# Kernel tuning notes

Measured on AMD Instinct MI355X. Metric: run time of the kernel, lower is better.

The kernel has to match this reference:

```python
import jax, jax.numpy as jnp
import numpy as np

N_NODES = 100000
N_EDGES = 1600000
N_GRAPHS = 1024
DIM_IN = 128
DIM_SELF = 16
BN_EPS = 1e-5


def _bn(x, gamma, beta):
    # training-mode BatchNorm1d over dim 0 (biased variance, as torch uses for normalization)
    m = jnp.mean(x, axis=0)
    v = jnp.mean((x - m) ** 2, axis=0)
    return gamma * (x - m) * jax.lax.rsqrt(v + BN_EPS) + beta


def _mlp(x, W1, b1, g, b, W2, b2):
    h = x @ W1 + b1
    h = jax.nn.relu(_bn(h, g, b))
    return h @ W2 + b2


def _gin(h, src, dst, W1, b1, g, b, W2, b2):
    # GINConv with eps=0: (1+eps)*h + sum over in-neighbors, then MLP
    agg = jax.ops.segment_sum(h[src], dst, num_segments=N_NODES)
    return _mlp(h + agg, W1, b1, g, b, W2, b2)


def setup_inputs() -> dict:
    key = jax.random.key(0)
    ks = jax.random.split(key, 16)

    def lin(k, fan_in, fan_out):
        bound = 1.0 / np.sqrt(fan_in)
        k1, k2 = jax.random.split(k)
        W = jax.random.uniform(k1, (fan_in, fan_out), jnp.float32, -bound, bound)
        b = jax.random.uniform(k2, (fan_out,), jnp.float32, -bound, bound)
        return W, b

    inp = {}
    inp['feat'] = jax.random.normal(ks[0], (N_NODES, DIM_IN), jnp.float32)
    inp['self_feat'] = jax.random.normal(ks[1], (N_GRAPHS, DIM_SELF), jnp.float32)
    inp['edge_src'] = jax.random.randint(ks[2], (N_EDGES,), 0, N_NODES, jnp.int32)
    inp['edge_dst'] = jax.random.randint(ks[3], (N_EDGES,), 0, N_NODES, jnp.int32)
    inp['node2graph'] = jnp.sort(jax.random.randint(ks[4], (N_NODES,), 0, N_GRAPHS, jnp.int32))

    inp['g1_W1'], inp['g1_b1'] = lin(ks[5], DIM_IN, 100)
    inp['g1_gamma'] = jnp.ones((100,), jnp.float32)
    inp['g1_beta'] = jnp.zeros((100,), jnp.float32)
    inp['g1_W2'], inp['g1_b2'] = lin(ks[6], 100, 100)

    inp['g2_W1'], inp['g2_b1'] = lin(ks[7], 100, 20)
    inp['g2_gamma'] = jnp.ones((20,), jnp.float32)
    inp['g2_beta'] = jnp.zeros((20,), jnp.float32)
    inp['g2_W2'], inp['g2_b2'] = lin(ks[8], 20, 20)

    inp['fc1_W'], inp['fc1_b'] = lin(ks[9], 20 * DIM_SELF, 32)
    inp['bn1_gamma'] = jnp.ones((32,), jnp.float32)
    inp['bn1_beta'] = jnp.zeros((32,), jnp.float32)
    inp['fc2_W'], inp['fc2_b'] = lin(ks[10], 32, 8)
    inp['bn2_gamma'] = jnp.ones((8,), jnp.float32)
    inp['bn2_beta'] = jnp.zeros((8,), jnp.float32)
    inp['fc3_W'], inp['fc3_b'] = lin(ks[11], 8, 1)
    return inp


def reference(feat, self_feat,
              g1_W1, g1_b1, g1_gamma, g1_beta, g1_W2, g1_b2,
              g2_W1, g2_b1, g2_gamma, g2_beta, g2_W2, g2_b2,
              fc1_W, fc1_b, bn1_gamma, bn1_beta,
              fc2_W, fc2_b, bn2_gamma, bn2_beta,
              fc3_W, fc3_b,
              edge_src, edge_dst, node2graph):
    h = _gin(feat, edge_src, edge_dst, g1_W1, g1_b1, g1_gamma, g1_beta, g1_W2, g1_b2)
    h = jax.nn.relu(h)
    h = _gin(h, edge_src, edge_dst, g2_W1, g2_b1, g2_gamma, g2_beta, g2_W2, g2_b2)
    h = jax.nn.relu(h)  # [N, 20]

    # dgl.mean_nodes: per-graph mean of node features
    sums = jax.ops.segment_sum(h, node2graph, num_segments=N_GRAPHS)  # [B, 20]
    cnts = jax.ops.segment_sum(jnp.ones((N_NODES,), h.dtype), node2graph, num_segments=N_GRAPHS)
    hg = sums / jnp.maximum(cnts, 1.0)[:, None]

    # kronecker fusion: bmm([B,20,1],[B,1,dim_self]) -> flatten
    kron = jnp.einsum('bi,bj->bij', hg, self_feat).reshape(N_GRAPHS, -1)  # [B, 20*dim_self]

    out = jax.nn.relu(_bn(kron @ fc1_W + fc1_b, bn1_gamma, bn1_beta))
    # dropout(0.3) is identity in eval mode
    out = jax.nn.relu(_bn(out @ fc2_W + fc2_b, bn2_gamma, bn2_beta))
    out = out @ fc3_W + fc3_b  # [B, dim_out]
    return out
```

## Files before the change

### kernel.cpp

```cpp
#include <hip/hip_runtime.h>

#define NN 100000
#define NE 1600000
#define NG 1024
#define DIN 128
#define D1 100
#define D2 20
#define DSELF 16
#define BN_EPS 1e-5f

#define NB 391
#define NBLK 782
#define EPB 2048
#define RAWCAP 5120
#define NAGG2 4000
#define NF1 25
#define NF2 40
#define APITCH 136

typedef unsigned int uint;
typedef unsigned short ushort;
typedef __attribute__((ext_vector_type(8))) short bfv8;
typedef __attribute__((ext_vector_type(4))) float fv4;

__device__ inline float bflo(uint x) { return __uint_as_float(x << 16); }
__device__ inline float bfhi(uint x) { return __uint_as_float(x & 0xffff0000u); }
__device__ inline uint packbf2(float a, float b) {
    uint ua = __float_as_uint(a), ub = __float_as_uint(b);
    ua += 0x7fffu + ((ua >> 16) & 1u);
    ub += 0x7fffu + ((ub >> 16) & 1u);
    return (ua >> 16) | (ub & 0xffff0000u);
}
__device__ inline ushort bfr(float x) {
    uint u = __float_as_uint(x);
    u += 0x7fffu + ((u >> 16) & 1u);
    return (ushort)(u >> 16);
}

__global__ __launch_bounds__(256) void k_gemm1(const float* __restrict__ feat,
                                               const float* __restrict__ W1,
                                               ushort* __restrict__ z1bf) {
    __shared__ __align__(16) char smem[64 * APITCH * 2 + 112 * APITCH * 2];
    ushort* Al = (ushort*)smem;
    ushort* Bt = (ushort*)(smem + 64 * APITCH * 2);
    int t = threadIdx.x;
    int row0 = blockIdx.x * 64;
#pragma unroll
    for (int i = 0; i < 8; i++) {
        int p = i * 256 + t;
        int r = p >> 5, cq = p & 31;
        int row = row0 + r; if (row >= NN) row = NN - 1;
        float4 v = *(const float4*)(feat + (size_t)row * DIN + cq * 4);
        ushort* dst = Al + r * APITCH + 4 * cq;
        dst[0] = bfr(v.x); dst[1] = bfr(v.y); dst[2] = bfr(v.z); dst[3] = bfr(v.w);
    }
    for (int p = t; p < 12800; p += 256) {
        int k = p / 100, n = p % 100;
        Bt[n * APITCH + k] = bfr(W1[p]);
    }
    __syncthreads();
    int w = __builtin_amdgcn_readfirstlane(t >> 6);
    int l = t & 63;
    int m16 = l & 15, quad = l >> 4;
    fv4 acc[7];
#pragma unroll
    for (int nt = 0; nt < 7; nt++) acc[nt] = (fv4){0.f, 0.f, 0.f, 0.f};
    const ushort* arow = Al + (w * 16 + m16) * APITCH;
#pragma unroll
    for (int kk = 0; kk < 4; kk++) {
        int kb = kk * 32 + quad * 8;
        bfv8 a = *(const bfv8*)(arow + kb);
#pragma unroll
        for (int nt = 0; nt < 7; nt++) {
            bfv8 b = *(const bfv8*)(Bt + (nt * 16 + m16) * APITCH + kb);
            acc[nt] = __builtin_amdgcn_mfma_f32_16x16x32_bf16(a, b, acc[nt], 0, 0, 0);
        }
    }
    __syncthreads();
    float* Ep = (float*)smem;
#pragma unroll
    for (int nt = 0; nt < 7; nt++) {
        int n = nt * 16 + m16;
        if (n < 100) {
#pragma unroll
            for (int rix = 0; rix < 4; rix++)
                Ep[(w * 16 + quad * 4 + rix) * 101 + n] = acc[nt][rix];
        }
    }
    __syncthreads();
#pragma unroll
    for (int i = 0; i < 13; i++) {
        int p = i * 256 + t;
        if (p < 3200) {
            int rr = p / 50, cc = 2 * (p % 50);
            int row = row0 + rr;
            if (row < NN) {
                float v0 = Ep[rr * 101 + cc], v1 = Ep[rr * 101 + cc + 1];
                *(uint*)(z1bf + (size_t)row * 128 + cc) = packbf2(v0, v1);
            }
        }
    }
}

__global__ __launch_bounds__(256) void k_csrA1(const int* __restrict__ dst,
                                               int* __restrict__ pbcount) {
    __shared__ int h[NB];
    int t = threadIdx.x, blk = blockIdx.x;
    for (int i = t; i < NB; i += 256) h[i] = 0;
    __syncthreads();
    int e0 = blk * EPB + t;
#pragma unroll
    for (int i = 0; i < 8; i++) {
        int e = e0 + i * 256;
        if (e < NE) atomicAdd(&h[dst[e] >> 8], 1);
    }
    __syncthreads();
    for (int i = t; i < NB; i += 256) pbcount[i * NBLK + blk] = h[i];
}

__global__ __launch_bounds__(1024) void k_csrS1(int* __restrict__ pbcount,
                                                int* __restrict__ btot) {
    __shared__ int s[1024];
    int t = threadIdx.x, b = blockIdx.x;
    int v = (t < NBLK) ? pbcount[b * NBLK + t] : 0;
    s[t] = v;
    __syncthreads();
    for (int off = 1; off < 1024; off <<= 1) {
        int x = (t >= off) ? s[t - off] : 0;
        __syncthreads();
        s[t] += x;
        __syncthreads();
    }
    if (t < NBLK) pbcount[b * NBLK + t] = s[t] - v;
    if (t == 1023) btot[b] = s[t];
}

__global__ __launch_bounds__(256) void k_csrA2(const int* __restrict__ src,
                                               const int* __restrict__ dst,
                                               const int* __restrict__ pbexcl,
                                               const int* __restrict__ btot,
                                               int* __restrict__ ebase_g,
                                               uint* __restrict__ gbuf) {
    __shared__ int cur[NB];
    __shared__ int sa[512], sb[512];
    int t = threadIdx.x, blk = blockIdx.x;
    int o0 = (t < NB) ? btot[t] : 0;
    int o1 = (t + 256 < NB) ? btot[t + 256] : 0;
    sa[t] = o0; sa[t + 256] = o1;
    __syncthreads();
    int* sp = sa; int* dp = sb;
    for (int off = 1; off < 512; off <<= 1) {
        dp[t] = sp[t] + ((t >= off) ? sp[t - off] : 0);
        int i2 = t + 256;
        dp[i2] = sp[i2] + ((i2 >= off) ? sp[i2 - off] : 0);
        __syncthreads();
        int* tmp = sp; sp = dp; dp = tmp;
    }
    if (t < NB)       cur[t]       = (sp[t] - o0) + pbexcl[t * NBLK + blk];
    if (t + 256 < NB) cur[t + 256] = (sp[t + 256] - o1) + pbexcl[(t + 256) * NBLK + blk];
    if (blk == 0) {
        if (t < NB)       ebase_g[t]       = sp[t] - o0;
        if (t + 256 < NB) ebase_g[t + 256] = sp[t + 256] - o1;
        if (t == 0)       ebase_g[NB]      = sp[NB - 1];
    }
    __syncthreads();
    int e0 = blk * EPB + t;
#pragma unroll
    for (int i = 0; i < 8; i++) {
        int e = e0 + i * 256;
        if (e < NE) {
            int d = dst[e];
            int b = d >> 8;
            int pos = atomicAdd(&cur[b], 1);
            gbuf[pos] = (uint)src[e] | ((uint)(d & 255) << 17);
        }
    }
}

__global__ __launch_bounds__(256) void k_csrB(const uint* __restrict__ gbuf,
                                              const int* __restrict__ ebase,
                                              int* __restrict__ deg,
                                              int* __restrict__ offs,
                                              int* __restrict__ srcS) {
    __shared__ uint raw[RAWCAP];
    __shared__ int srt[RAWCAP];
    __shared__ int pref[256], cur[256];
    int t = threadIdx.x, b = blockIdx.x;
    int e0 = ebase[b], e1 = ebase[b + 1];
    int cnt = e1 - e0; if (cnt > RAWCAP) cnt = RAWCAP;
    cur[t] = 0;
    for (int i = t; i < cnt; i += 256) raw[i] = gbuf[e0 + i];
    __syncthreads();
    for (int i = t; i < cnt; i += 256) atomicAdd(&cur[raw[i] >> 17], 1);
    __syncthreads();
    int v = cur[t];
    pref[t] = v;
    __syncthreads();
    for (int off = 1; off < 256; off <<= 1) {
        int x = (t >= off) ? pref[t - off] : 0;
        __syncthreads();
        pref[t] += x;
        __syncthreads();
    }
    int excl = pref[t] - v;
    int node = b * 256 + t;
    if (node < NN) { deg[node] = v; offs[node] = e0 + excl; }
    cur[t] = excl;
    __syncthreads();
    for (int i = t; i < cnt; i += 256) {
        uint p = raw[i];
        int lpos = atomicAdd(&cur[p >> 17], 1);
        srt[lpos] = (int)(p & 0x1FFFFu);
    }
    __syncthreads();
    for (int i = t; i < cnt; i += 256) srcS[e0 + i] = srt[i];
}

__global__ __launch_bounds__(256) void k_agg1(const ushort* __restrict__ z1bf,
                                              const int* __restrict__ offs,
                                              const int* __restrict__ deg,
                                              const int* __restrict__ srcS,
                                              ushort* __restrict__ u1b) {
    int wq = __builtin_amdgcn_readfirstlane(threadIdx.x >> 6);
    int l = threadIdx.x & 63;
    int n = blockIdx.x * 4 + wq;
    if (n >= NN) return;
    int d = deg[n], base = offs[n];
    bool act = l < 50;
    const ushort* zc = z1bf + 2 * l;
    float a0 = 0.f, a1 = 0.f, b0 = 0.f, b1 = 0.f;
    float c0 = 0.f, c1 = 0.f, e0 = 0.f, e1 = 0.f;
    int i = 0;
    for (; i + 8 <= d; i += 8) {
        int s0 = srcS[base + i],     s1 = srcS[base + i + 1];
        int s2 = srcS[base + i + 2], s3 = srcS[base + i + 3];
        int s4 = srcS[base + i + 4], s5 = srcS[base + i + 5];
        int s6 = srcS[base + i + 6], s7 = srcS[base + i + 7];
        if (act) {
            uint x0 = *(const uint*)(zc + (size_t)s0 * 128);
            uint x1 = *(const uint*)(zc + (size_t)s1 * 128);
            uint x2 = *(const uint*)(zc + (size_t)s2 * 128);
            uint x3 = *(const uint*)(zc + (size_t)s3 * 128);
            uint x4 = *(const uint*)(zc + (size_t)s4 * 128);
            uint x5 = *(const uint*)(zc + (size_t)s5 * 128);
            uint x6 = *(const uint*)(zc + (size_t)s6 * 128);
            uint x7 = *(const uint*)(zc + (size_t)s7 * 128);
            a0 += bflo(x0); a1 += bfhi(x0);
            b0 += bflo(x1); b1 += bfhi(x1);
            c0 += bflo(x2); c1 += bfhi(x2);
            e0 += bflo(x3); e1 += bfhi(x3);
            a0 += bflo(x4); a1 += bfhi(x4);
            b0 += bflo(x5); b1 += bfhi(x5);
            c0 += bflo(x6); c1 += bfhi(x6);
            e0 += bflo(x7); e1 += bfhi(x7);
        }
    }
    for (; i + 2 <= d; i += 2) {
        int s0 = srcS[base + i], s1 = srcS[base + i + 1];
        if (act) {
            uint x0 = *(const uint*)(zc + (size_t)s0 * 128);
            uint x1 = *(const uint*)(zc + (size_t)s1 * 128);
            a0 += bflo(x0); a1 += bfhi(x0);
            b0 += bflo(x1); b1 += bfhi(x1);
        }
    }
    if (i < d) {
        int s0 = srcS[base + i];
        if (act) {
            uint x0 = *(const uint*)(zc + (size_t)s0 * 128);
            a0 += bflo(x0); a1 += bfhi(x0);
        }
    }
    if (act) {
        uint xs = *(const uint*)(zc + (size_t)n * 128);
        float r0 = (a0 + b0) + (c0 + e0) + bflo(xs);
        float r1 = (a1 + b1) + (c1 + e1) + bfhi(xs);
        *(uint*)(u1b + (size_t)n * 100 + 2 * l) = packbf2(r0, r1);
    }
}

__global__ __launch_bounds__(256) void k_bnstat100(const ushort* __restrict__ u1b,
                                                   float* __restrict__ pb) {
    __shared__ float ls[10][100], lq[10][100];
    int t = threadIdx.x;
    int r0 = blockIdx.x * 200;
    int r1 = r0 + 200; if (r1 > NN) r1 = NN;
    if (t < 250) {
        int sub = t / 25, q = t % 25;
        float4 S = make_float4(0, 0, 0, 0), Q = make_float4(0, 0, 0, 0);
        for (int r = r0 + sub; r < r1; r += 10) {
            uint2 x = *(const uint2*)(u1b + (size_t)r * 100 + 4 * q);
            float v0 = bflo(x.x), v1 = bfhi(x.x), v2 = bflo(x.y), v3 = bfhi(x.y);
            S.x += v0; S.y += v1; S.z += v2; S.w += v3;
            Q.x = fmaf(v0, v0, Q.x); Q.y = fmaf(v1, v1, Q.y);
            Q.z = fmaf(v2, v2, Q.z); Q.w = fmaf(v3, v3, Q.w);
        }
        ls[sub][4 * q + 0] = S.x; ls[sub][4 * q + 1] = S.y;
        ls[sub][4 * q + 2] = S.z; ls[sub][4 * q + 3] = S.w;
        lq[sub][4 * q + 0] = Q.x; lq[sub][4 * q + 1] = Q.y;
        lq[sub][4 * q + 2] = Q.z; lq[sub][4 * q + 3] = Q.w;
    }
    __syncthreads();
    if (t < 100) {
        float S = 0.f, Q = 0.f;
#pragma unroll
        for (int s = 0; s < 10; s++) { S += ls[s][t]; Q += lq[s][t]; }
        pb[blockIdx.x * 200 + t] = S;
        pb[blockIdx.x * 200 + 100 + t] = Q;
    }
}

__global__ __launch_bounds__(256) void k_fold100(const float* __restrict__ pb,
                                                 float* __restrict__ pbf) {
    __shared__ float ls[4000];
    int t = threadIdx.x, b = blockIdx.x;
    for (int i = t; i < 4000; i += 256) ls[i] = pb[b * 4000 + i];
    __syncthreads();
    if (t < 200) {
        float S = 0.f;
#pragma unroll
        for (int j = 0; j < 20; j++) S += ls[j * 200 + t];
        pbf[b * 200 + t] = S;
    }
}

__global__ __launch_bounds__(512) void k_bnfin100(const float* __restrict__ pbf,
                                                  const float* __restrict__ gamma,
                                                  const float* __restrict__ beta,
                                                  float* __restrict__ sc,
                                                  float* __restrict__ sh) {
    __shared__ float ls[4][100], lq[4][100];
    int t = threadIdx.x;
    if (t < 400) {
        int sub = t / 100, c = t % 100;
        float S = 0.f, Q = 0.f;
        for (int b = sub; b < NF1; b += 4) {
            S += pbf[b * 200 + c];
            Q += pbf[b * 200 + 100 + c];
        }
        ls[sub][c] = S; lq[sub][c] = Q;
    }
    __syncthreads();
    if (t < 100) {
        float S = ls[0][t] + ls[1][t] + ls[2][t] + ls[3][t];
        float Q = lq[0][t] + lq[1][t] + lq[2][t] + lq[3][t];
        float mean = S * (1.f / NN);
        float var = Q * (1.f / NN) - mean * mean;
        float inv = rsqrtf(var + BN_EPS);
        float s = gamma[t] * inv;
        sc[t] = s;
        sh[t] = beta[t] - mean * s;
    }
}

__global__ __launch_bounds__(256) void k_m2(const ushort* __restrict__ u1b,
                                            const float* __restrict__ sc,
                                            const float* __restrict__ sh,
                                            const float* __restrict__ W2,
                                            const float* __restrict__ b2,
                                            const float* __restrict__ W1p,
                                            ushort* __restrict__ z2bf) {
    __shared__ float Xs[100 * 65];
    int t = threadIdx.x;
    int row0 = blockIdx.x * 64;
#pragma unroll
    for (int i = 0; i < 13; i++) {
        int p = i * 256 + t;
        if (p < 3200) {
            int r = p / 50, c = 2 * (p % 50);
            int row = row0 + r; if (row >= NN) row = NN - 1;
            uint x = *(const uint*)(u1b + (size_t)row * 100 + c);
            Xs[c * 65 + r] = fmaxf(bflo(x) * sc[c] + sh[c], 0.f);
            Xs[(c + 1) * 65 + r] = fmaxf(bfhi(x) * sc[c + 1] + sh[c + 1], 0.f);
        }
    }
    __syncthreads();
    int cg = __builtin_amdgcn_readfirstlane(t >> 6);
    int r = t & 63;
    int j0 = cg * 25;
    float H[25];
#pragma unroll
    for (int m = 0; m < 25; m++) H[m] = 0.f;
    for (int k = 0; k < D1; k++) {
        float a = Xs[k * 65 + r];
        const float* wr = W2 + k * D1 + j0;
#pragma unroll
        for (int m = 0; m < 25; m++) H[m] = fmaf(a, wr[m], H[m]);
    }
#pragma unroll
    for (int m = 0; m < 25; m++) H[m] = fmaxf(H[m] + b2[j0 + m], 0.f);
    float pz[20];
#pragma unroll
    for (int c = 0; c < 20; c++) pz[c] = 0.f;
#pragma unroll
    for (int m = 0; m < 25; m++) {
        const float* wp = W1p + (j0 + m) * D2;
#pragma unroll
        for (int c = 0; c < 20; c++) pz[c] = fmaf(H[m], wp[c], pz[c]);
    }
    __syncthreads();
    float* red = Xs;
#pragma unroll
    for (int c = 0; c < 20; c++) red[t * 20 + c] = pz[c];
    __syncthreads();
#pragma unroll
    for (int i = 0; i < 3; i++) {
        int p = i * 256 + t;
        if (p < 640) {
            int rr = p / 10, c2 = 2 * (p % 10);
            int row = row0 + rr;
            if (row < NN) {
                float v0 = red[rr * 20 + c2] + red[(64 + rr) * 20 + c2] +
                           red[(128 + rr) * 20 + c2] + red[(192 + rr) * 20 + c2];
                float v1 = red[rr * 20 + c2 + 1] + red[(64 + rr) * 20 + c2 + 1] +
                           red[(128 + rr) * 20 + c2 + 1] + red[(192 + rr) * 20 + c2 + 1];
                *(uint*)(z2bf + (size_t)row * 32 + c2) = packbf2(v0, v1);
            }
        }
    }
}

__global__ __launch_bounds__(256) void k_agg2(const ushort* __restrict__ z2bf,
                                              const int* __restrict__ offs,
                                              const int* __restrict__ deg,
                                              const int* __restrict__ srcS,
                                              float* __restrict__ u2,
                                              float* __restrict__ pb) {
    __shared__ float ls[500], lq[500];
    int t = threadIdx.x;
    int n = blockIdx.x * 25 + t / 10;
    int c2 = 2 * (t % 10);
    float r0 = 0.f, r1 = 0.f;
    if (t < 250 && n < NN) {
        int d = deg[n], base = offs[n];
        const ushort* zc = z2bf + c2;
        float a0 = 0.f, a1 = 0.f, b0 = 0.f, b1 = 0.f;
        int i = 0;
        for (; i + 2 <= d; i += 2) {
            uint x0 = *(const uint*)(zc + (size_t)srcS[base + i] * 32);
            uint x1 = *(const uint*)(zc + (size_t)srcS[base + i + 1] * 32);
            a0 += bflo(x0); a1 += bfhi(x0);
            b0 += bflo(x1); b1 += bfhi(x1);
        }
        if (i < d) {
            uint x0 = *(const uint*)(zc + (size_t)srcS[base + i] * 32);
            a0 += bflo(x0); a1 += bfhi(x0);
        }
        uint xs = *(const uint*)(zc + (size_t)n * 32);
        r0 = a0 + b0 + bflo(xs);
        r1 = a1 + b1 + bfhi(xs);
        *(float2*)(u2 + (size_t)n * D2 + c2) = make_float2(r0, r1);
    }
    if (t < 250) {
        int idx = (t / 10) * 20 + c2;
        ls[idx] = r0;     lq[idx] = r0 * r0;
        ls[idx + 1] = r1; lq[idx + 1] = r1 * r1;
    }
    __syncthreads();
    if (t < 20) {
        float S = 0.f, Q = 0.f;
#pragma unroll
        for (int j = 0; j < 25; j++) { S += ls[j * 20 + t]; Q += lq[j * 20 + t]; }
        pb[blockIdx.x * 40 + t] = S;
        pb[blockIdx.x * 40 + 20 + t] = Q;
    }
}

__global__ __launch_bounds__(256) void k_fold20(const float* __restrict__ pb,
                                                float* __restrict__ pbf) {
    __shared__ float ls[4000];
    int t = threadIdx.x, b = blockIdx.x;
    for (int i = t; i < 4000; i += 256) ls[i] = pb[b * 4000 + i];
    __syncthreads();
    if (t < 40) {
        float S = 0.f;
#pragma unroll
        for (int j = 0; j < 100; j++) S += ls[j * 40 + t];
        pbf[b * 40 + t] = S;
    }
}

__global__ __launch_bounds__(512) void k_bnfin20(const float* __restrict__ pbf,
                                                 const float* __restrict__ gamma,
                                                 const float* __restrict__ beta,
                                                 float* __restrict__ sc,
                                                 float* __restrict__ sh) {
    __shared__ float ls[25][20], lq[25][20];
    int t = threadIdx.x;
    if (t < 500) {
        int sub = t / 20, c = t % 20;
        float S = 0.f, Q = 0.f;
        for (int b = sub; b < NF2; b += 25) {
            S += pbf[b * 40 + c];
            Q += pbf[b * 40 + 20 + c];
        }
        ls[sub][c] = S; lq[sub][c] = Q;
    }
    __syncthreads();
    if (t < 20) {
        float S = 0.f, Q = 0.f;
#pragma unroll
        for (int s = 0; s < 25; s++) { S += ls[s][t]; Q += lq[s][t]; }
        float mean = S * (1.f / NN);
        float var = Q * (1.f / NN) - mean * mean;
        float inv = rsqrtf(var + BN_EPS);
        float s = gamma[t] * inv;
        sc[t] = s;
        sh[t] = beta[t] - mean * s;
    }
}

__global__ __launch_bounds__(256) void k_m3(const float* __restrict__ u2,
                                            const float* __restrict__ sc,
                                            const float* __restrict__ sh,
                                            const float* __restrict__ W2p,
                                            const float* __restrict__ b2p,
                                            float* __restrict__ h2) {
    int row = blockIdx.x * 256 + threadIdx.x;
    if (row >= NN) return;
    float ya[20];
    const float4* up = (const float4*)(u2 + (size_t)row * D2);
#pragma unroll
    for (int i = 0; i < 5; i++) {
        float4 v = up[i];
        float4 S = *(const float4*)(sc + 4 * i);
        float4 H = *(const float4*)(sh + 4 * i);
        ya[4 * i + 0] = fmaxf(v.x * S.x + H.x, 0.f);
        ya[4 * i + 1] = fmaxf(v.y * S.y + H.y, 0.f);
        ya[4 * i + 2] = fmaxf(v.z * S.z + H.z, 0.f);
        ya[4 * i + 3] = fmaxf(v.w * S.w + H.w, 0.f);
    }
    float hrow[D2];
#pragma unroll
    for (int j = 0; j < D2; j++) {
        float h = b2p[j];
#pragma unroll
        for (int k = 0; k < D2; k++) h = fmaf(ya[k], W2p[k * D2 + j], h);
        hrow[j] = fmaxf(h, 0.f);
    }
    float* hr = h2 + (size_t)row * D2;
#pragma unroll
    for (int c = 0; c < D2; c += 4) {
        float4 o; o.x = hrow[c]; o.y = hrow[c + 1]; o.z = hrow[c + 2]; o.w = hrow[c + 3];
        *(float4*)(hr + c) = o;
    }
}

__global__ __launch_bounds__(256) void k_pool(const float* __restrict__ h2,
                                              const int* __restrict__ n2g,
                                              float* __restrict__ hg) {
    int wq = __builtin_amdgcn_readfirstlane(threadIdx.x >> 6);
    int l = threadIdx.x & 63;
    int g = blockIdx.x * 4 + wq;
    if (g >= NG) return;
    int lo = 0, hi = NN;
    while (lo < hi) { int mid = (lo + hi) >> 1; if (n2g[mid] < g) lo = mid + 1; else hi = mid; }
    int s0 = lo;
    hi = NN;
    while (lo < hi) { int mid = (lo + hi) >> 1; if (n2g[mid] < g + 1) lo = mid + 1; else hi = mid; }
    int s1 = lo;
    float a = 0.f;
    if (l < 60) {
        int rg = l / 20, c = l % 20;
        for (int n = s0 + rg; n < s1; n += 3) a += h2[(size_t)n * D2 + c];
    }
    float v1 = __shfl(a, l + 20, 64);
    float v2 = __shfl(a, l + 40, 64);
    if (l < 20) {
        float cnt = (float)(s1 - s0);
        hg[g * D2 + l] = (a + v1 + v2) / fmaxf(cnt, 1.f);
    }
}

__global__ void k_head1(const float* __restrict__ hg, const float* __restrict__ sf,
                        const float* __restrict__ fc1W, float* __restrict__ a1) {
    int b = blockIdx.x * 8 + threadIdx.x / 32;
    int c = threadIdx.x % 32;
    if (b >= NG) return;
    const float* hgb = hg + b * D2;
    const float* sfb = sf + b * DSELF;
    float acc = 0.f;
    for (int i = 0; i < D2; i++) {
        float hi = hgb[i];
#pragma unroll
        for (int j = 0; j < DSELF; j++)
            acc += hi * sfb[j] * fc1W[(i * DSELF + j) * 32 + c];
    }
    a1[b * 32 + c] = acc;
}

__global__ __launch_bounds__(1024) void k_head2(
    const float* __restrict__ a1, const float* __restrict__ g1,
    const float* __restrict__ be1, const float* __restrict__ fc2W,
    const float* __restrict__ g2, const float* __restrict__ be2,
    const float* __restrict__ fc3W, const float* __restrict__ fc3b,
    float* __restrict__ out) {
    int t = threadIdx.x;
    int lane = t & 63, w = t >> 6;
    __shared__ float s1[16][32], s2[16][32];
    __shared__ float sc[32], sh[32], sc2[8], sh2[8];
    float x[32];
    const float4* ap = (const float4*)(a1 + t * 32);
#pragma unroll
    for (int i = 0; i < 8; i++) {
        float4 v = ap[i];
        x[4 * i] = v.x; x[4 * i + 1] = v.y; x[4 * i + 2] = v.z; x[4 * i + 3] = v.w;
    }
#pragma unroll
    for (int c = 0; c < 32; c++) {
        float v = x[c], q = v * v;
        for (int o = 32; o > 0; o >>= 1) {
            v += __shfl_down(v, o, 64);
            q += __shfl_down(q, o, 64);
        }
        if (lane == 0) { s1[w][c] = v; s2[w][c] = q; }
    }
    __syncthreads();
    if (t < 32) {
        float s = 0.f, q = 0.f;
        for (int ww = 0; ww < 16; ww++) { s += s1[ww][t]; q += s2[ww][t]; }
        float mean = s * (1.f / NG);
        float var = q * (1.f / NG) - mean * mean;
        float inv = rsqrtf(var + BN_EPS);
        float scl = g1[t] * inv;
        sc[t] = scl;
        sh[t] = be1[t] - mean * scl;
    }
    __syncthreads();
#pragma unroll
    for (int c = 0; c < 32; c++) x[c] = fmaxf(x[c] * sc[c] + sh[c], 0.f);
    float y[8];
#pragma unroll
    for (int p = 0; p < 8; p++) {
        float a = 0.f;
#pragma unroll
        for (int c = 0; c < 32; c++) a += x[c] * fc2W[c * 8 + p];
        y[p] = a;
    }
    __syncthreads();
#pragma unroll
    for (int p = 0; p < 8; p++) {
        float v = y[p], q = v * v;
        for (int o = 32; o > 0; o >>= 1) {
            v += __shfl_down(v, o, 64);
            q += __shfl_down(q, o, 64);
        }
        if (lane == 0) { s1[w][p] = v; s2[w][p] = q; }
    }
    __syncthreads();
    if (t < 8) {
        float s = 0.f, q = 0.f;
        for (int ww = 0; ww < 16; ww++) { s += s1[ww][t]; q += s2[ww][t]; }
        float mean = s * (1.f / NG);
        float var = q * (1.f / NG) - mean * mean;
        float inv = rsqrtf(var + BN_EPS);
        float scl = g2[t] * inv;
        sc2[t] = scl;
        sh2[t] = be2[t] - mean * scl;
    }
    __syncthreads();
    float o = fc3b[0];
#pragma unroll
    for (int p = 0; p < 8; p++) {
        float yy = fmaxf(y[p] * sc2[p] + sh2[p], 0.f);
        o += yy * fc3W[p];
    }
    out[t] = o;
}

extern "C" void kernel_launch(void* const* d_in, const int* in_sizes, int n_in,
                              void* d_out, int out_size, void* d_ws, size_t ws_size,
                              hipStream_t stream) {
    const float* feat    = (const float*)d_in[0];
    const float* sf      = (const float*)d_in[1];
    const int*   esrc    = (const int*)d_in[2];
    const int*   edst    = (const int*)d_in[3];
    const int*   n2g     = (const int*)d_in[4];
    const float* g1W1    = (const float*)d_in[5];
    const float* g1gam   = (const float*)d_in[7];
    const float* g1bet   = (const float*)d_in[8];
    const float* g1W2    = (const float*)d_in[9];
    const float* g1b2    = (const float*)d_in[10];
    const float* g2W1    = (const float*)d_in[11];
    const float* g2gam   = (const float*)d_in[13];
    const float* g2bet   = (const float*)d_in[14];
    const float* g2W2    = (const float*)d_in[15];
    const float* g2b2    = (const float*)d_in[16];
    const float* fc1W    = (const float*)d_in[17];
    const float* hbn1g   = (const float*)d_in[19];
    const float* hbn1b   = (const float*)d_in[20];
    const float* fc2W    = (const float*)d_in[21];
    const float* hbn2g   = (const float*)d_in[23];
    const float* hbn2b   = (const float*)d_in[24];
    const float* fc3W    = (const float*)d_in[25];
    const float* fc3b    = (const float*)d_in[26];
    float* out = (float*)d_out;

    char* w = (char*)d_ws;
    size_t off = 0;
    auto alloc = [&](size_t bytes) -> char* {
        char* p = w + off;
        off += (bytes + 15) & ~(size_t)15;
        return p;
    };
    char* regA = alloc((size_t)NN * 128 * 2);
    ushort* z1bf = (ushort*)regA;
    ushort* z2bf = (ushort*)regA;
    float*  u2   = (float*)(regA + 6400000);
    float*  h2   = (float*)(regA + 14400000);
    ushort* u1b  = (ushort*)alloc((size_t)NN * 100 * 2);
    int*   pbcnt = (int*)alloc((size_t)NB * NBLK * 4);
    int*   btot  = (int*)alloc(NB * 4);
    int*   ebase = (int*)alloc((NB + 1) * 4);
    uint*  gbuf  = (uint*)alloc((size_t)NE * 4);
    int*   deg   = (int*)alloc(NN * 4);
    int*   offs  = (int*)alloc(NN * 4);
    int*   srcS  = (int*)alloc((size_t)NE * 4);
    float* pb1   = (float*)alloc(500 * 200 * 4);
    float* pb1f  = (float*)alloc(NF1 * 200 * 4);
    float* pb2   = (float*)alloc((size_t)NAGG2 * 40 * 4);
    float* pb2f  = (float*)alloc(NF2 * 40 * 4);
    float* sc1   = (float*)alloc(D1 * 4);
    float* sh1   = (float*)alloc(D1 * 4);
    float* sc2   = (float*)alloc(D2 * 4);
    float* sh2   = (float*)alloc(D2 * 4);
    float* hg    = (float*)alloc(NG * D2 * 4);
    float* a1    = (float*)alloc(NG * 32 * 4);
    (void)in_sizes; (void)n_in; (void)out_size; (void)ws_size;

    k_gemm1<<<(NN + 63) / 64, 256, 0, stream>>>(feat, g1W1, z1bf);

    k_csrA1<<<NBLK, 256, 0, stream>>>(edst, pbcnt);
    k_csrS1<<<NB, 1024, 0, stream>>>(pbcnt, btot);
    k_csrA2<<<NBLK, 256, 0, stream>>>(esrc, edst, pbcnt, btot, ebase, gbuf);
    k_csrB<<<NB, 256, 0, stream>>>(gbuf, ebase, deg, offs, srcS);

    k_agg1<<<(NN + 3) / 4, 256, 0, stream>>>(z1bf, offs, deg, srcS, u1b);
    k_bnstat100<<<500, 256, 0, stream>>>(u1b, pb1);
    k_fold100<<<NF1, 256, 0, stream>>>(pb1, pb1f);
    k_bnfin100<<<1, 512, 0, stream>>>(pb1f, g1gam, g1bet, sc1, sh1);
    k_m2<<<(NN + 63) / 64, 256, 0, stream>>>(u1b, sc1, sh1, g1W2, g1b2, g2W1, z2bf);

    k_agg2<<<NAGG2, 256, 0, stream>>>(z2bf, offs, deg, srcS, u2, pb2);
    k_fold20<<<NF2, 256, 0, stream>>>(pb2, pb2f);
    k_bnfin20<<<1, 512, 0, stream>>>(pb2f, g2gam, g2bet, sc2, sh2);
    k_m3<<<(NN + 255) / 256, 256, 0, stream>>>(u2, sc2, sh2, g2W2, g2b2, h2);

    k_pool<<<(NG + 3) / 4, 256, 0, stream>>>(h2, n2g, hg);
    k_head1<<<NG / 8, 256, 0, stream>>>(hg, sf, fc1W, a1);
    k_head2<<<1, 1024, 0, stream>>>(a1, hbn1g, hbn1b, fc2W, hbn2g, hbn2b, fc3W, fc3b, out);
}
```

Measured before the change: 430.8 us.

## Fuse BN statistics into aggregation kernels via replicated atomic partials, pack z1 rows

The layer-1 BatchNorm statistics (sum and sum of squares) are now computed inside the aggregation kernel from the fp32 results, with 1024-thread blocks reducing across 16 node-waves and atomically adding into 64 replicated partial buffers. The layer-2 statistics use the same replicated atomics, so the separate bnstat and fold kernels and their launches go away. The partial buffers are zeroed by block 0 of the preceding GEMM kernels. The z1 intermediate row pitch shrinks from 128 to 100 bf16 values, which cuts gather footprint. The risks are float-atomic nondeterminism, the zeroing relying on launch ordering, and layer-1 statistics now taken on unrounded fp32 values rather than bf16-rounded ones.

```diff
diff --git a/kernel.cpp b/kernel.cpp
--- a/kernel.cpp
+++ b/kernel.cpp
@@ -14,8 +14,7 @@
 #define EPB 2048
 #define RAWCAP 5120
 #define NAGG2 4000
-#define NF1 25
-#define NF2 40
+#define NREP 64
 #define APITCH 136
 
 typedef unsigned int uint;
@@ -39,11 +38,15 @@
 
 __global__ __launch_bounds__(256) void k_gemm1(const float* __restrict__ feat,
                                                const float* __restrict__ W1,
-                                               ushort* __restrict__ z1bf) {
+                                               ushort* __restrict__ z1bf,
+                                               float* __restrict__ pb1r) {
     __shared__ __align__(16) char smem[64 * APITCH * 2 + 112 * APITCH * 2];
     ushort* Al = (ushort*)smem;
     ushort* Bt = (ushort*)(smem + 64 * APITCH * 2);
     int t = threadIdx.x;
+    if (blockIdx.x == 0) {
+        for (int i = t; i < NREP * 200; i += 256) pb1r[i] = 0.f;
+    }
     int row0 = blockIdx.x * 64;
 #pragma unroll
     for (int i = 0; i < 8; i++) {
@@ -96,7 +99,7 @@
             int row = row0 + rr;
             if (row < NN) {
                 float v0 = Ep[rr * 101 + cc], v1 = Ep[rr * 101 + cc + 1];
-                *(uint*)(z1bf + (size_t)row * 128 + cc) = packbf2(v0, v1);
+                *(uint*)(z1bf + (size_t)row * 100 + cc) = packbf2(v0, v1);
             }
         }
     }
@@ -216,17 +219,20 @@
     for (int i = t; i < cnt; i += 256) srcS[e0 + i] = srt[i];
 }
 
-__global__ __launch_bounds__(256) void k_agg1(const ushort* __restrict__ z1bf,
-                                              const int* __restrict__ offs,
-                                              const int* __restrict__ deg,
-                                              const int* __restrict__ srcS,
-                                              ushort* __restrict__ u1b) {
-    int wq = __builtin_amdgcn_readfirstlane(threadIdx.x >> 6);
-    int l = threadIdx.x & 63;
-    int n = blockIdx.x * 4 + wq;
-    if (n >= NN) return;
-    int d = deg[n], base = offs[n];
-    bool act = l < 50;
+__global__ __launch_bounds__(1024) void k_agg1(const ushort* __restrict__ z1bf,
+                                               const int* __restrict__ offs,
+                                               const int* __restrict__ deg,
+                                               const int* __restrict__ srcS,
+                                               ushort* __restrict__ u1b,
+                                               float* __restrict__ pb1r) {
+    __shared__ float part[16][200];
+    int t = threadIdx.x;
+    int wq = __builtin_amdgcn_readfirstlane(t >> 6);
+    int l = t & 63;
+    int n = blockIdx.x * 16 + wq;
+    int d = 0, base = 0;
+    if (n < NN) { d = deg[n]; base = offs[n]; }
+    bool act = (l < 50) && (n < NN);
     const ushort* zc = z1bf + 2 * l;
     float a0 = 0.f, a1 = 0.f, b0 = 0.f, b1 = 0.f;
     float c0 = 0.f, c1 = 0.f, e0 = 0.f, e1 = 0.f;
@@ -237,14 +243,14 @@
         int s4 = srcS[base + i + 4], s5 = srcS[base + i + 5];
         int s6 = srcS[base + i + 6], s7 = srcS[base + i + 7];
         if (act) {
-            uint x0 = *(const uint*)(zc + (size_t)s0 * 128);
-            uint x1 = *(const uint*)(zc + (size_t)s1 * 128);
-            uint x2 = *(const uint*)(zc + (size_t)s2 * 128);
-            uint x3 = *(const uint*)(zc + (size_t)s3 * 128);
-            uint x4 = *(const uint*)(zc + (size_t)s4 * 128);
-            uint x5 = *(const uint*)(zc + (size_t)s5 * 128);
-            uint x6 = *(const uint*)(zc + (size_t)s6 * 128);
-            uint x7 = *(const uint*)(zc + (size_t)s7 * 128);
+            uint x0 = *(const uint*)(zc + (size_t)s0 * 100);
+            uint x1 = *(const uint*)(zc + (size_t)s1 * 100);
+            uint x2 = *(const uint*)(zc + (size_t)s2 * 100);
+            uint x3 = *(const uint*)(zc + (size_t)s3 * 100);
+            uint x4 = *(const uint*)(zc + (size_t)s4 * 100);
+            uint x5 = *(const uint*)(zc + (size_t)s5 * 100);
+            uint x6 = *(const uint*)(zc + (size_t)s6 * 100);
+            uint x7 = *(const uint*)(zc + (size_t)s7 * 100);
             a0 += bflo(x0); a1 += bfhi(x0);
             b0 += bflo(x1); b1 += bfhi(x1);
             c0 += bflo(x2); c1 += bfhi(x2);
@@ -258,8 +264,8 @@
     for (; i + 2 <= d; i += 2) {
         int s0 = srcS[base + i], s1 = srcS[base + i + 1];
         if (act) {
-            uint x0 = *(const uint*)(zc + (size_t)s0 * 128);
-            uint x1 = *(const uint*)(zc + (size_t)s1 * 128);
+            uint x0 = *(const uint*)(zc + (size_t)s0 * 100);
+            uint x1 = *(const uint*)(zc + (size_t)s1 * 100);
             a0 += bflo(x0); a1 += bfhi(x0);
             b0 += bflo(x1); b1 += bfhi(x1);
         }
@@ -267,83 +273,46 @@
     if (i < d) {
         int s0 = srcS[base + i];
         if (act) {
-            uint x0 = *(const uint*)(zc + (size_t)s0 * 128);
+            uint x0 = *(const uint*)(zc + (size_t)s0 * 100);
             a0 += bflo(x0); a1 += bfhi(x0);
         }
     }
+    float r0 = 0.f, r1 = 0.f;
     if (act) {
-        uint xs = *(const uint*)(zc + (size_t)n * 128);
-        float r0 = (a0 + b0) + (c0 + e0) + bflo(xs);
-        float r1 = (a1 + b1) + (c1 + e1) + bfhi(xs);
+        uint xs = *(const uint*)(zc + (size_t)n * 100);
+        r0 = (a0 + b0) + (c0 + e0) + bflo(xs);
+        r1 = (a1 + b1) + (c1 + e1) + bfhi(xs);
         *(uint*)(u1b + (size_t)n * 100 + 2 * l) = packbf2(r0, r1);
     }
-}
-
-__global__ __launch_bounds__(256) void k_bnstat100(const ushort* __restrict__ u1b,
-                                                   float* __restrict__ pb) {
-    __shared__ float ls[10][100], lq[10][100];
-    int t = threadIdx.x;
-    int r0 = blockIdx.x * 200;
-    int r1 = r0 + 200; if (r1 > NN) r1 = NN;
-    if (t < 250) {
-        int sub = t / 25, q = t % 25;
-        float4 S = make_float4(0, 0, 0, 0), Q = make_float4(0, 0, 0, 0);
-        for (int r = r0 + sub; r < r1; r += 10) {
-            uint2 x = *(const uint2*)(u1b + (size_t)r * 100 + 4 * q);
-            float v0 = bflo(x.x), v1 = bfhi(x.x), v2 = bflo(x.y), v3 = bfhi(x.y);
-            S.x += v0; S.y += v1; S.z += v2; S.w += v3;
-            Q.x = fmaf(v0, v0, Q.x); Q.y = fmaf(v1, v1, Q.y);
-            Q.z = fmaf(v2, v2, Q.z); Q.w = fmaf(v3, v3, Q.w);
-        }
-        ls[sub][4 * q + 0] = S.x; ls[sub][4 * q + 1] = S.y;
-        ls[sub][4 * q + 2] = S.z; ls[sub][4 * q + 3] = S.w;
-        lq[sub][4 * q + 0] = Q.x; lq[sub][4 * q + 1] = Q.y;
-        lq[sub][4 * q + 2] = Q.z; lq[sub][4 * q + 3] = Q.w;
-    }
-    __syncthreads();
-    if (t < 100) {
-        float S = 0.f, Q = 0.f;
-#pragma unroll
-        for (int s = 0; s < 10; s++) { S += ls[s][t]; Q += lq[s][t]; }
-        pb[blockIdx.x * 200 + t] = S;
-        pb[blockIdx.x * 200 + 100 + t] = Q;
-    }
-}
-
-__global__ __launch_bounds__(256) void k_fold100(const float* __restrict__ pb,
-                                                 float* __restrict__ pbf) {
-    __shared__ float ls[4000];
-    int t = threadIdx.x, b = blockIdx.x;
-    for (int i = t; i < 4000; i += 256) ls[i] = pb[b * 4000 + i];
+    if (l < 50) {
+        part[wq][2 * l] = r0;            part[wq][2 * l + 1] = r1;
+        part[wq][100 + 2 * l] = r0 * r0; part[wq][100 + 2 * l + 1] = r1 * r1;
+    }
     __syncthreads();
     if (t < 200) {
-        float S = 0.f;
-#pragma unroll
-        for (int j = 0; j < 20; j++) S += ls[j * 200 + t];
-        pbf[b * 200 + t] = S;
-    }
-}
-
-__global__ __launch_bounds__(512) void k_bnfin100(const float* __restrict__ pbf,
+        float s = 0.f;
+#pragma unroll
+        for (int w2 = 0; w2 < 16; w2++) s += part[w2][t];
+        atomicAdd(&pb1r[(blockIdx.x & (NREP - 1)) * 200 + t], s);
+    }
+}
+
+__global__ __launch_bounds__(256) void k_bnfin100(const float* __restrict__ pb1r,
                                                   const float* __restrict__ gamma,
                                                   const float* __restrict__ beta,
                                                   float* __restrict__ sc,
                                                   float* __restrict__ sh) {
-    __shared__ float ls[4][100], lq[4][100];
+    __shared__ float red[200];
     int t = threadIdx.x;
-    if (t < 400) {
-        int sub = t / 100, c = t % 100;
-        float S = 0.f, Q = 0.f;
-        for (int b = sub; b < NF1; b += 4) {
-            S += pbf[b * 200 + c];
-            Q += pbf[b * 200 + 100 + c];
-        }
-        ls[sub][c] = S; lq[sub][c] = Q;
+    if (t < 200) {
+        float s = 0.f;
+#pragma unroll 8
+        for (int r = 0; r < NREP; r++) s += pb1r[r * 200 + t];
+        red[t] = s;
     }
     __syncthreads();
     if (t < 100) {
-        float S = ls[0][t] + ls[1][t] + ls[2][t] + ls[3][t];
-        float Q = lq[0][t] + lq[1][t] + lq[2][t] + lq[3][t];
+        float S = red[t], Q = red[100 + t];
         float mean = S * (1.f / NN);
         float var = Q * (1.f / NN) - mean * mean;
         float inv = rsqrtf(var + BN_EPS);
@@ -359,9 +328,13 @@
                                             const float* __restrict__ W2,
                                             const float* __restrict__ b2,
                                             const float* __restrict__ W1p,
-                                            ushort* __restrict__ z2bf) {
+                                            ushort* __restrict__ z2bf,
+                                            float* __restrict__ pb2r) {
     __shared__ float Xs[100 * 65];
     int t = threadIdx.x;
+    if (blockIdx.x == 0) {
+        for (int i = t; i < NREP * 40; i += 256) pb2r[i] = 0.f;
+    }
     int row0 = blockIdx.x * 64;
 #pragma unroll
     for (int i = 0; i < 13; i++) {
@@ -425,7 +398,7 @@
                                               const int* __restrict__ deg,
                                               const int* __restrict__ srcS,
                                               float* __restrict__ u2,
-                                              float* __restrict__ pb) {
+                                              float* __restrict__ pb2r) {
     __shared__ float ls[500], lq[500];
     int t = threadIdx.x;
     int n = blockIdx.x * 25 + t / 10;
@@ -461,46 +434,28 @@
         float S = 0.f, Q = 0.f;
 #pragma unroll
         for (int j = 0; j < 25; j++) { S += ls[j * 20 + t]; Q += lq[j * 20 + t]; }
-        pb[blockIdx.x * 40 + t] = S;
-        pb[blockIdx.x * 40 + 20 + t] = Q;
-    }
-}
-
-__global__ __launch_bounds__(256) void k_fold20(const float* __restrict__ pb,
-                                                float* __restrict__ pbf) {
-    __shared__ float ls[4000];
-    int t = threadIdx.x, b = blockIdx.x;
-    for (int i = t; i < 4000; i += 256) ls[i] = pb[b * 4000 + i];
-    __syncthreads();
+        int rep = (blockIdx.x & (NREP - 1)) * 40;
+        atomicAdd(&pb2r[rep + t], S);
+        atomicAdd(&pb2r[rep + 20 + t], Q);
+    }
+}
+
+__global__ __launch_bounds__(64) void k_bnfin20(const float* __restrict__ pb2r,
+                                                const float* __restrict__ gamma,
+                                                const float* __restrict__ beta,
+                                                float* __restrict__ sc,
+                                                float* __restrict__ sh) {
+    __shared__ float red[40];
+    int t = threadIdx.x;
     if (t < 40) {
-        float S = 0.f;
-#pragma unroll
-        for (int j = 0; j < 100; j++) S += ls[j * 40 + t];
-        pbf[b * 40 + t] = S;
-    }
-}
-
-__global__ __launch_bounds__(512) void k_bnfin20(const float* __restrict__ pbf,
-                                                 const float* __restrict__ gamma,
-                                                 const float* __restrict__ beta,
-                                                 float* __restrict__ sc,
-                                                 float* __restrict__ sh) {
-    __shared__ float ls[25][20], lq[25][20];
-    int t = threadIdx.x;
-    if (t < 500) {
-        int sub = t / 20, c = t % 20;
-        float S = 0.f, Q = 0.f;
-        for (int b = sub; b < NF2; b += 25) {
-            S += pbf[b * 40 + c];
-            Q += pbf[b * 40 + 20 + c];
-        }
-        ls[sub][c] = S; lq[sub][c] = Q;
+        float s = 0.f;
+#pragma unroll 8
+        for (int r = 0; r < NREP; r++) s += pb2r[r * 40 + t];
+        red[t] = s;
     }
     __syncthreads();
     if (t < 20) {
-        float S = 0.f, Q = 0.f;
-#pragma unroll
-        for (int s = 0; s < 25; s++) { S += ls[s][t]; Q += lq[s][t]; }
+        float S = red[t], Q = red[20 + t];
         float mean = S * (1.f / NN);
         float var = Q * (1.f / NN) - mean * mean;
         float inv = rsqrtf(var + BN_EPS);
@@ -716,10 +671,8 @@
     int*   deg   = (int*)alloc(NN * 4);
     int*   offs  = (int*)alloc(NN * 4);
     int*   srcS  = (int*)alloc((size_t)NE * 4);
-    float* pb1   = (float*)alloc(500 * 200 * 4);
-    float* pb1f  = (float*)alloc(NF1 * 200 * 4);
-    float* pb2   = (float*)alloc((size_t)NAGG2 * 40 * 4);
-    float* pb2f  = (float*)alloc(NF2 * 40 * 4);
+    float* pb1r  = (float*)alloc((size_t)NREP * 200 * 4);
+    float* pb2r  = (float*)alloc((size_t)NREP * 40 * 4);
     float* sc1   = (float*)alloc(D1 * 4);
     float* sh1   = (float*)alloc(D1 * 4);
     float* sc2   = (float*)alloc(D2 * 4);
@@ -728,22 +681,19 @@
     float* a1    = (float*)alloc(NG * 32 * 4);
     (void)in_sizes; (void)n_in; (void)out_size; (void)ws_size;
 
-    k_gemm1<<<(NN + 63) / 64, 256, 0, stream>>>(feat, g1W1, z1bf);
+    k_gemm1<<<(NN + 63) / 64, 256, 0, stream>>>(feat, g1W1, z1bf, pb1r);
 
     k_csrA1<<<NBLK, 256, 0, stream>>>(edst, pbcnt);
     k_csrS1<<<NB, 1024, 0, stream>>>(pbcnt, btot);
     k_csrA2<<<NBLK, 256, 0, stream>>>(esrc, edst, pbcnt, btot, ebase, gbuf);
     k_csrB<<<NB, 256, 0, stream>>>(gbuf, ebase, deg, offs, srcS);
 
-    k_agg1<<<(NN + 3) / 4, 256, 0, stream>>>(z1bf, offs, deg, srcS, u1b);
-    k_bnstat100<<<500, 256, 0, stream>>>(u1b, pb1);
-    k_fold100<<<NF1, 256, 0, stream>>>(pb1, pb1f);
-    k_bnfin100<<<1, 512, 0, stream>>>(pb1f, g1gam, g1bet, sc1, sh1);
-    k_m2<<<(NN + 63) / 64, 256, 0, stream>>>(u1b, sc1, sh1, g1W2, g1b2, g2W1, z2bf);
-
-    k_agg2<<<NAGG2, 256, 0, stream>>>(z2bf, offs, deg, srcS, u2, pb2);
-    k_fold20<<<NF2, 256, 0, stream>>>(pb2, pb2f);
-    k_bnfin20<<<1, 512, 0, stream>>>(pb2f, g2gam, g2bet, sc2, sh2);
+    k_agg1<<<NN / 16, 1024, 0, stream>>>(z1bf, offs, deg, srcS, u1b, pb1r);
+    k_bnfin100<<<1, 256, 0, stream>>>(pb1r, g1gam, g1bet, sc1, sh1);
+    k_m2<<<(NN + 63) / 64, 256, 0, stream>>>(u1b, sc1, sh1, g1W2, g1b2, g2W1, z2bf, pb2r);
+
+    k_agg2<<<NAGG2, 256, 0, stream>>>(z2bf, offs, deg, srcS, u2, pb2r);
+    k_bnfin20<<<1, 64, 0, stream>>>(pb2r, g2gam, g2bet, sc2, sh2);
     k_m3<<<(NN + 255) / 256, 256, 0, stream>>>(u2, sc2, sh2, g2W2, g2b2, h2);
 
     k_pool<<<(NG + 3) / 4, 256, 0, stream>>>(h2, n2g, hg);
```

New measurement: 429.6 us. No clear change (-0.3%).
